# Performance work log

Hardware: AMD Instinct MI355X
Metric: run time of the kernel (lower is better)

The kernel has to match this reference:

```python
import jax, jax.numpy as jnp
import numpy as np
from jax import lax

NPOINT = 1024
RADIUS = 0.4
NSAMPLE = 32
BN_EPS = 1e-5


def _square_distance(src, dst):
    # src [B,S,3], dst [B,N,3] -> [B,S,N]
    d = -2.0 * jnp.einsum('bsc,bnc->bsn', src, dst)
    d = d + jnp.sum(src ** 2, -1)[:, :, None]
    d = d + jnp.sum(dst ** 2, -1)[:, None, :]
    return d


def _farthest_point_sample(xyz, npoint):
    # xyz [B,N,3] -> int32 indices [B,npoint]
    B, N, _ = xyz.shape
    # deterministic start at index 0 (torch uses randint; math is otherwise identical)
    init_far = jnp.zeros((B,), dtype=jnp.int32)
    init_dist = jnp.full((B, N), 1e10, dtype=xyz.dtype)

    def step(carry, _):
        distance, farthest = carry
        centroid = jnp.take_along_axis(xyz, farthest[:, None, None], axis=1)  # [B,1,3]
        dist = jnp.sum((xyz - centroid) ** 2, -1)  # [B,N]
        distance = jnp.minimum(distance, dist)
        new_far = jnp.argmax(distance, axis=-1).astype(jnp.int32)
        return (distance, new_far), farthest

    (_, _), cents = lax.scan(step, (init_dist, init_far), None, length=npoint)
    return cents.T  # [B, npoint]


def _query_ball_point(radius, nsample, xyz, new_xyz):
    # xyz [B,N,3], new_xyz [B,S,3] -> idx [B,S,nsample]
    B, N, _ = xyz.shape
    sqr = _square_distance(new_xyz, xyz)  # [B,S,N]
    ar = jnp.arange(N, dtype=jnp.int32)
    gi = jnp.where(sqr > radius * radius, N, ar[None, None, :])
    gi = jnp.sort(gi, axis=-1)[:, :, :nsample]
    first = gi[:, :, :1]
    return jnp.where(gi == N, first, gi)


def setup_inputs() -> dict:
    key = jax.random.key(0)
    ks = jax.random.split(key, 8)
    B, N = 16, 4096
    inp = {
        'xyz': jax.random.normal(ks[0], (B, 3, N), jnp.float32),
        'points': jax.random.normal(ks[1], (B, 6, N), jnp.float32),
    }
    dims = [(64, 9), (64, 64), (128, 64)]
    for i, (o, c) in enumerate(dims):
        inp[f'w{i}'] = jax.random.normal(ks[2 + i], (o, c), jnp.float32) * 0.05
        inp[f'b{i}'] = jnp.zeros((o,), jnp.float32)
        inp[f'g{i}'] = jnp.ones((o,), jnp.float32)
        inp[f'beta{i}'] = jnp.zeros((o,), jnp.float32)
    return inp


def reference(xyz, points, w0, b0, g0, beta0, w1, b1, g1, beta1, w2, b2, g2, beta2):
    # xyz [B,3,N], points [B,6,N]
    xyz_t = jnp.transpose(xyz, (0, 2, 1))      # [B,N,3]
    pts_t = jnp.transpose(points, (0, 2, 1))   # [B,N,6]
    B, N, _ = xyz_t.shape
    S, ns = NPOINT, NSAMPLE

    fps_idx = _farthest_point_sample(xyz_t, S)                 # [B,S]
    new_xyz = jnp.take_along_axis(xyz_t, fps_idx[:, :, None], axis=1)  # [B,S,3]
    idx = _query_ball_point(RADIUS, ns, xyz_t, new_xyz)        # [B,S,ns]
    flat = idx.reshape(B, S * ns, 1)
    g_xyz = jnp.take_along_axis(xyz_t, flat, axis=1).reshape(B, S, ns, 3)
    g_xyz = g_xyz - new_xyz[:, :, None, :]                     # grouped_xyz_norm
    g_pts = jnp.take_along_axis(pts_t, flat, axis=1).reshape(B, S, ns, -1)
    feat = jnp.concatenate([g_xyz, g_pts], axis=-1)            # [B,S,ns,9]

    # shared MLP: 1x1 conv + BatchNorm (training-mode batch stats) + ReLU
    for w, b, g, be in ((w0, b0, g0, beta0), (w1, b1, g1, beta1), (w2, b2, g2, beta2)):
        h = jnp.einsum('bsnc,oc->bsno', feat, w) + b
        mu = jnp.mean(h, axis=(0, 1, 2))
        var = jnp.var(h, axis=(0, 1, 2))
        feat = jax.nn.relu((h - mu) * lax.rsqrt(var + BN_EPS) * g + be)

    new_points = jnp.max(feat, axis=2)                         # max over nsample -> [B,S,Cout]
    return (jnp.transpose(new_xyz, (0, 2, 1)), jnp.transpose(new_points, (0, 2, 1)))
```

## Files before the change

### kernel.cpp

```cpp
#include <hip/hip_runtime.h>
#include <hip/hip_bf16.h>
#include <stdint.h>

#define NB 16
#define NP 4096
#define NSP 1024
#define KNN 32
#define PTOT (NB*NSP*KNN)
#define NTILES (PTOT/16)

typedef __attribute__((ext_vector_type(8))) short short8;
typedef __attribute__((ext_vector_type(4))) float f32x4;
typedef __attribute__((ext_vector_type(2))) float f32x2;

__device__ __forceinline__ float fadd_(float a,float b){return __fadd_rn(a,b);}
__device__ __forceinline__ float fmul_(float a,float b){return __fmul_rn(a,b);}
__device__ __forceinline__ float fsub_(float a,float b){return __fsub_rn(a,b);}

__device__ __forceinline__ float bf2f(unsigned short u){
    unsigned int x = ((unsigned int)u) << 16; float f; __builtin_memcpy(&f,&x,4); return f;
}
__device__ __forceinline__ unsigned short f2bf(float f){
    unsigned int x; __builtin_memcpy(&x,&f,4);
    x = x + 0x7fffu + ((x>>16)&1u);
    return (unsigned short)(x>>16);
}

template<int CTRL>
__device__ __forceinline__ float dpp_fmax_step(float v){
    int d = __builtin_amdgcn_update_dpp(0, __float_as_int(v), CTRL, 0xF, 0xF, true);
    return fmaxf(v, __int_as_float(d));
}

__global__ __launch_bounds__(256,1) void fps_kernel(const float* __restrict__ xyz,
    int* __restrict__ fps_idx)
{
    const int b = blockIdx.x, tid = threadIdx.x;
    const int lane = tid & 63, wv = tid >> 6;
    const float* xb = xyz + (size_t)b*3*NP;
    __shared__ float4 sp[NP];
    __shared__ unsigned long long slots[2][4];
    f32x2 px[8], py[8], pz[8], pd2[8];
    const int base = tid*16;
#pragma unroll
    for (int j=0;j<16;j+=4){
        float4 vx = *(const float4*)(xb + base + j);
        float4 vy = *(const float4*)(xb + NP + base + j);
        float4 vz = *(const float4*)(xb + 2*NP + base + j);
        px[j/2]   = (f32x2){vx.x,vx.y}; px[j/2+1] = (f32x2){vx.z,vx.w};
        py[j/2]   = (f32x2){vy.x,vy.y}; py[j/2+1] = (f32x2){vy.z,vy.w};
        pz[j/2]   = (f32x2){vz.x,vz.y}; pz[j/2+1] = (f32x2){vz.z,vz.w};
        sp[base+j+0] = make_float4(vx.x,vy.x,vz.x,0.f);
        sp[base+j+1] = make_float4(vx.y,vy.y,vz.y,0.f);
        sp[base+j+2] = make_float4(vx.z,vy.z,vz.z,0.f);
        sp[base+j+3] = make_float4(vx.w,vy.w,vz.w,0.f);
        pd2[j/2]   = (f32x2){1e10f,1e10f};
        pd2[j/2+1] = (f32x2){1e10f,1e10f};
    }
    __syncthreads();
    int far = 0;
    float cx, cy, cz;
    { float4 c0 = sp[0]; cx=c0.x; cy=c0.y; cz=c0.z; }
    for (int s=0;s<NSP;s++){
        if (tid==0) fps_idx[b*NSP+s] = far;
        f32x2 bm2 = (f32x2){-1.f,-1.f};
        {
#pragma clang fp contract(off)
            const f32x2 cx2 = (f32x2){cx,cx}, cy2 = (f32x2){cy,cy}, cz2 = (f32x2){cz,cz};
#pragma unroll
            for (int k=0;k<8;k++){
                f32x2 dx = px[k]-cx2, dy = py[k]-cy2, dz = pz[k]-cz2;
                f32x2 d  = (dx*dx + dy*dy) + dz*dz;
                pd2[k] = __builtin_elementwise_min(pd2[k], d);
                bm2    = __builtin_elementwise_max(bm2, pd2[k]);
            }
        }
        float bd = fmaxf(bm2.x, bm2.y);
        float m = bd;
        m = dpp_fmax_step<0x111>(m);
        m = dpp_fmax_step<0x112>(m);
        m = dpp_fmax_step<0x114>(m);
        m = dpp_fmax_step<0x118>(m);
        m = dpp_fmax_step<0x142>(m);
        m = dpp_fmax_step<0x143>(m);
        const float wm = __int_as_float(__builtin_amdgcn_readlane(__float_as_int(m), 63));
        int il = 0;
#pragma unroll
        for (int k=7;k>=0;k--){
            if (pd2[k].y == wm) il = 2*k+1;
            if (pd2[k].x == wm) il = 2*k;
        }
        unsigned long long wmask = __ballot(bd == wm);
        int L = __ffsll(wmask) - 1;
        int widx = __builtin_amdgcn_readlane(base + il, L);
        unsigned long long key = ((unsigned long long)__float_as_uint(wm) << 32)
                               | (unsigned int)(NP-1-widx);
        if (lane==0) slots[s&1][wv] = key;
        __syncthreads();
        {
            const unsigned long long* sl = slots[s&1];
            unsigned long long a0 = sl[0], a1 = sl[1], a2 = sl[2], a3 = sl[3];
            unsigned long long m0 = a0>a1?a0:a1, m1 = a2>a3?a2:a3;
            unsigned long long mm = m0>m1?m0:m1;
            far = NP-1-(int)(mm & 0xFFFFFFFFu);
        }
        float4 c = sp[far]; cx=c.x; cy=c.y; cz=c.z;
    }
}

__global__ void centroid_kernel(const float* __restrict__ xyz, const int* __restrict__ fps_idx,
    float* __restrict__ new_xyz, float* __restrict__ out0)
{
    int t = blockIdx.x*256 + threadIdx.x;
    if (t >= NB*NSP) return;
    int b = t>>10, s = t&1023;
    int id = fps_idx[t];
    const float* xb = xyz + (size_t)b*3*NP;
    float x=xb[id], y=xb[NP+id], z=xb[2*NP+id];
    float* nz = new_xyz + (size_t)t*3;
    nz[0]=x; nz[1]=y; nz[2]=z;
    out0[(size_t)b*3*NSP + s]         = x;
    out0[(size_t)b*3*NSP + NSP + s]   = y;
    out0[(size_t)b*3*NSP + 2*NSP + s] = z;
}

__global__ __launch_bounds__(256,1) void ball_gather_kernel(const float* __restrict__ xyz,
    const float* __restrict__ pts, const float* __restrict__ new_xyz,
    unsigned short* __restrict__ feat)
{
    const int lane = threadIdx.x & 63, wv = threadIdx.x >> 6;
    const int center = blockIdx.x*4 + wv;
    const int b = center >> 10;
    const float* xb = xyz + (size_t)b*3*NP;
    const float* pb = pts + (size_t)b*6*NP;
    const float* nz = new_xyz + (size_t)center*3;
    const float cx=nz[0], cy=nz[1], cz=nz[2];
    const float src2 = fadd_(fadd_(fmul_(cx,cx),fmul_(cy,cy)),fmul_(cz,cz));
    const float R2 = (float)(0.4*0.4);
    __shared__ int slots[4][32];
    int total = 0;
    for (int c0=0;c0<NP;c0+=64){
        const int i = c0 + lane;
        float x=xb[i], y=xb[NP+i], z=xb[2*NP+i];
        float dot  = fadd_(fadd_(fmul_(cx,x),fmul_(cy,y)),fmul_(cz,z));
        float dst2 = fadd_(fadd_(fmul_(x,x),fmul_(y,y)),fmul_(z,z));
        float d = fadd_(fadd_(fmul_(-2.0f,dot), src2), dst2);
        bool pred = !(d > R2);
        unsigned long long m = __ballot(pred);
        int pos = total + (int)__popcll(m & ((1ull<<lane)-1ull));
        if (pred && pos < 32) slots[wv][pos] = i;
        total += (int)__popcll(m);
        if (total >= 32) break;
    }
    const int nvalid = total < 32 ? total : 32;
    const int n = lane & 31;
    const int idx = slots[wv][ (n < nvalid) ? n : 0 ];
    unsigned short* fr = feat + (size_t)center*KNN*32 + (size_t)n*32;
    if (lane < 32){
        float gx = fsub_(xb[idx], cx), gy = fsub_(xb[NP+idx], cy), gz = fsub_(xb[2*NP+idx], cz);
        float p0=pb[idx], p1=pb[NP+idx], p2=pb[2*NP+idx], p3=pb[3*NP+idx], p4=pb[4*NP+idx];
        short8 v;
        v[0]=(short)f2bf(gx); v[1]=(short)f2bf(gy); v[2]=(short)f2bf(gz);
        v[3]=(short)f2bf(p0); v[4]=(short)f2bf(p1); v[5]=(short)f2bf(p2);
        v[6]=(short)f2bf(p3); v[7]=(short)f2bf(p4);
        *(short8*)fr = v;
    } else {
        float p5 = pb[5*NP+idx];
        short8 v = (short8){0,0,0,0,0,0,0,0};
        v[0]=(short)f2bf(p5);
        *(short8*)(fr+8)  = v;
        short8 z8 = (short8){0,0,0,0,0,0,0,0};
        *(short8*)(fr+16) = z8;
        *(short8*)(fr+24) = z8;
    }
}

template<int KT,int OT,bool NORM_IN,bool STORE_H>
__global__ __launch_bounds__(256,1) void conv_kernel(const unsigned short* __restrict__ in,
    const unsigned short* __restrict__ wp, const float* __restrict__ bias,
    const float* __restrict__ nAB, unsigned short* __restrict__ h_out,
    double* __restrict__ stats)
{
    constexpr int K = KT*32, O = OT*16;
    const int lane = threadIdx.x & 63, wv = threadIdx.x >> 6;
    const int col = lane & 15, quad = lane >> 4;
    short8 bf[OT][KT];
#pragma unroll
    for (int t=0;t<OT;t++)
#pragma unroll
        for (int kt=0;kt<KT;kt++)
            bf[t][kt] = *(const short8*)(wp + (size_t)(t*16+col)*K + kt*32 + quad*8);
    float brow[OT];
#pragma unroll
    for (int t=0;t<OT;t++) brow[t] = bias[t*16+col];
    float nA[KT*8], nB[KT*8];
    if constexpr (NORM_IN){
#pragma unroll
        for (int kt=0;kt<KT;kt++)
#pragma unroll
            for (int j=0;j<8;j++){
                int c = kt*32+quad*8+j;
                nA[kt*8+j]=nAB[c]; nB[kt*8+j]=nAB[128+c];
            }
    }
    float ssum[OT], ssq[OT];
#pragma unroll
    for (int t=0;t<OT;t++){ ssum[t]=0.f; ssq[t]=0.f; }
    const int gw = blockIdx.x*4 + wv, nw = gridDim.x*4;
    for (int tile=gw; tile<NTILES; tile+=nw){
        const int row0 = tile*16;
        short8 af[KT];
#pragma unroll
        for (int kt=0;kt<KT;kt++){
            af[kt] = *(const short8*)(in + (size_t)(row0+col)*K + kt*32 + quad*8);
            if constexpr (NORM_IN){
#pragma unroll
                for (int j=0;j<8;j++){
                    float x = bf2f((unsigned short)af[kt][j]);
                    x = fmaxf(x*nA[kt*8+j]+nB[kt*8+j], 0.f);
                    af[kt][j] = (short)f2bf(x);
                }
            }
        }
        f32x4 acc[OT];
#pragma unroll
        for (int t=0;t<OT;t++) acc[t] = (f32x4){0.f,0.f,0.f,0.f};
#pragma unroll
        for (int kt=0;kt<KT;kt++)
#pragma unroll
            for (int t=0;t<OT;t++)
                acc[t] = __builtin_amdgcn_mfma_f32_16x16x32_bf16(af[kt], bf[t][kt], acc[t], 0,0,0);
#pragma unroll
        for (int t=0;t<OT;t++){
#pragma unroll
            for (int r=0;r<4;r++){
                float h = acc[t][r] + brow[t];
                if constexpr (STORE_H)
                    h_out[(size_t)(row0 + quad*4 + r)*O + t*16 + col] = f2bf(h);
                ssum[t] += h; ssq[t] = fmaf(h,h,ssq[t]);
            }
        }
    }
    __shared__ float bsum[128], bssq[128];
    for (int i=threadIdx.x;i<128;i+=256){ bsum[i]=0.f; bssq[i]=0.f; }
    __syncthreads();
#pragma unroll
    for (int t=0;t<OT;t++){
        float v = ssum[t]; v += __shfl_xor(v,16,64); v += __shfl_xor(v,32,64);
        float q = ssq[t];  q += __shfl_xor(q,16,64); q += __shfl_xor(q,32,64);
        if (quad==0){ atomicAdd(&bsum[t*16+col], v); atomicAdd(&bssq[t*16+col], q); }
    }
    __syncthreads();
    if ((int)threadIdx.x < O){
        const int slot = blockIdx.x & 7;
        atomicAdd(&stats[(size_t)(slot*2+0)*128 + threadIdx.x], (double)bsum[threadIdx.x]);
        atomicAdd(&stats[(size_t)(slot*2+1)*128 + threadIdx.x], (double)bssq[threadIdx.x]);
    }
}

__global__ void finalize_kernel(const double* __restrict__ stats, const float* __restrict__ g,
    const float* __restrict__ beta, float* __restrict__ AB, int O)
{
    int o = threadIdx.x;
    if (o >= O) return;
    double s=0.0, q=0.0;
#pragma unroll
    for (int slot=0;slot<8;slot++){
        s += stats[(size_t)(slot*2+0)*128+o];
        q += stats[(size_t)(slot*2+1)*128+o];
    }
    const double cnt = (double)PTOT;
    float mean = (float)(s/cnt);
    float var  = (float)(q/cnt - (s/cnt)*(s/cnt));
    float inv  = rsqrtf(var + 1e-5f);
    float A = g[o]*inv;
    AB[o] = A; AB[128+o] = beta[o] - mean*A;
}

__global__ __launch_bounds__(256,1) void conv_final_kernel(const unsigned short* __restrict__ in,
    const unsigned short* __restrict__ wp, const float* __restrict__ bias,
    const float* __restrict__ nABin, const float* __restrict__ nABout,
    float* __restrict__ out1)
{
    constexpr int KT=2, OT=8, K=64;
    const int lane = threadIdx.x & 63, wv = threadIdx.x >> 6;
    const int col = lane & 15, quad = lane >> 4;
    short8 bf[OT][KT];
#pragma unroll
    for (int t=0;t<OT;t++)
#pragma unroll
        for (int kt=0;kt<KT;kt++)
            bf[t][kt] = *(const short8*)(wp + (size_t)(t*16+col)*K + kt*32 + quad*8);
    float brow[OT], oA[OT], oB[OT];
#pragma unroll
    for (int t=0;t<OT;t++){
        brow[t] = bias[t*16+col];
        oA[t] = nABout[t*16+col];
        oB[t] = nABout[128+t*16+col];
    }
    float nA[16], nB[16];
#pragma unroll
    for (int kt=0;kt<2;kt++)
#pragma unroll
        for (int j=0;j<8;j++){
            int c = kt*32+quad*8+j;
            nA[kt*8+j]=nABin[c]; nB[kt*8+j]=nABin[128+c];
        }
    const int gw = blockIdx.x*4 + wv, nw = gridDim.x*4;
    for (int grp=gw; grp<NB*NSP; grp+=nw){
        float vmax[OT];
#pragma unroll
        for (int t=0;t<OT;t++) vmax[t]=0.f;
#pragma unroll
        for (int mt=0; mt<2; mt++){
            const int row0 = grp*32 + mt*16;
            short8 af[KT];
#pragma unroll
            for (int kt=0;kt<2;kt++){
                af[kt] = *(const short8*)(in + (size_t)(row0+col)*K + kt*32 + quad*8);
#pragma unroll
                for (int j=0;j<8;j++){
                    float x = bf2f((unsigned short)af[kt][j]);
                    x = fmaxf(x*nA[kt*8+j]+nB[kt*8+j], 0.f);
                    af[kt][j] = (short)f2bf(x);
                }
            }
            f32x4 acc[OT];
#pragma unroll
            for (int t=0;t<OT;t++) acc[t] = (f32x4){0.f,0.f,0.f,0.f};
#pragma unroll
            for (int kt=0;kt<2;kt++)
#pragma unroll
                for (int t=0;t<OT;t++)
                    acc[t] = __builtin_amdgcn_mfma_f32_16x16x32_bf16(af[kt], bf[t][kt], acc[t], 0,0,0);
#pragma unroll
            for (int t=0;t<OT;t++){
#pragma unroll
                for (int r=0;r<4;r++){
                    float h = acc[t][r] + brow[t];
                    float x = fmaxf(h*oA[t]+oB[t], 0.f);
                    vmax[t] = fmaxf(vmax[t], x);
                }
            }
        }
#pragma unroll
        for (int t=0;t<OT;t++){
            float v = vmax[t];
            v = fmaxf(v, __shfl_xor(v,16,64));
            v = fmaxf(v, __shfl_xor(v,32,64));
            if (quad==0){
                int o = t*16+col, bb = grp>>10, ss = grp&1023;
                out1[((size_t)bb*128+o)*NSP + ss] = v;
            }
        }
    }
}

__global__ void prep_kernel(const float* __restrict__ w0, const float* __restrict__ w1,
    const float* __restrict__ w2, unsigned short* __restrict__ wp0,
    unsigned short* __restrict__ wp1, unsigned short* __restrict__ wp2)
{
    int t = blockIdx.x*256 + threadIdx.x;
    if (t < 64*32){ int o=t>>5, c=t&31; wp0[t] = (c<9) ? f2bf(w0[o*9+c]) : (unsigned short)0; }
    if (t < 64*64)  wp1[t] = f2bf(w1[t]);
    if (t < 128*64) wp2[t] = f2bf(w2[t]);
}

extern "C" void kernel_launch(void* const* d_in, const int* in_sizes, int n_in,
                              void* d_out, int out_size, void* d_ws, size_t ws_size,
                              hipStream_t stream)
{
    (void)in_sizes; (void)n_in; (void)out_size; (void)ws_size;
    const float* xyz = (const float*)d_in[0];
    const float* pts = (const float*)d_in[1];
    const float* w0  = (const float*)d_in[2];
    const float* b0  = (const float*)d_in[3];
    const float* g0  = (const float*)d_in[4];
    const float* be0 = (const float*)d_in[5];
    const float* w1  = (const float*)d_in[6];
    const float* b1  = (const float*)d_in[7];
    const float* g1  = (const float*)d_in[8];
    const float* be1 = (const float*)d_in[9];
    const float* w2  = (const float*)d_in[10];
    const float* b2  = (const float*)d_in[11];
    const float* g2  = (const float*)d_in[12];
    const float* be2 = (const float*)d_in[13];

    char* ws = (char*)d_ws;
    size_t off = 0;
    auto alloc = [&](size_t sz)->char*{ char* p = ws + off; off = (off + sz + 255) & ~(size_t)255; return p; };
    int*            fps_idx = (int*)           alloc((size_t)NB*NSP*4);
    float*          new_xyz = (float*)         alloc((size_t)NB*NSP*3*4);
    unsigned short* wp0     = (unsigned short*)alloc(64*32*2);
    unsigned short* wp1     = (unsigned short*)alloc(64*64*2);
    unsigned short* wp2     = (unsigned short*)alloc(128*64*2);
    double*         stats   = (double*)        alloc((size_t)3*8*2*128*8);
    float*          AB0     = (float*)         alloc(256*4);
    float*          AB1     = (float*)         alloc(256*4);
    float*          AB2     = (float*)         alloc(256*4);
    unsigned short* feat    = (unsigned short*)alloc((size_t)PTOT*32*2);
    unsigned short* h0      = (unsigned short*)alloc((size_t)PTOT*64*2);
    unsigned short* h1      = (unsigned short*)alloc((size_t)PTOT*64*2);

    float* out0 = (float*)d_out;
    float* out1 = out0 + (size_t)NB*3*NSP;

    hipMemsetAsync(stats, 0, (size_t)3*8*2*128*8, stream);
    prep_kernel<<<32,256,0,stream>>>(w0,w1,w2,wp0,wp1,wp2);
    fps_kernel<<<NB,256,0,stream>>>(xyz, fps_idx);
    centroid_kernel<<<(NB*NSP+255)/256,256,0,stream>>>(xyz, fps_idx, new_xyz, out0);
    ball_gather_kernel<<<NB*NSP/4,256,0,stream>>>(xyz, pts, new_xyz, feat);
    conv_kernel<1,4,false,true><<<1024,256,0,stream>>>(feat, wp0, b0, nullptr, h0, stats);
    finalize_kernel<<<1,128,0,stream>>>(stats, g0, be0, AB0, 64);
    conv_kernel<2,4,true,true><<<1024,256,0,stream>>>(h0, wp1, b1, AB0, h1, stats + 2048);
    finalize_kernel<<<1,128,0,stream>>>(stats + 2048, g1, be1, AB1, 64);
    conv_kernel<2,8,true,false><<<1024,256,0,stream>>>(h1, wp2, b2, AB1, nullptr, stats + 4096);
    finalize_kernel<<<1,128,0,stream>>>(stats + 4096, g2, be2, AB2, 128);
    conv_final_kernel<<<2048,256,0,stream>>>(h1, wp2, b2, AB1, AB2, out1);
}
```

Measured before the change: 882.0 us.

## Carry winner coordinates through LDS slots in FPS instead of indexed LDS lookup

Each FPS iteration used to reduce the argmax key across waves and then do a dependent LDS read of the full point table to fetch the new centroid. Now every thread selects its local best point's coordinates from registers before the wave reduction. The winning lane writes its key and coordinates together to LDS, so the serial chain loses one dependent LDS load and the 64KB point table goes away. Per-iteration global stores of fps indices are buffered in LDS and written out at the end, at the cost of more register selects per iteration.

```diff
diff --git a/kernel.cpp b/kernel.cpp
--- a/kernel.cpp
+++ b/kernel.cpp
@@ -32,14 +32,27 @@
     return fmaxf(v, __int_as_float(d));
 }
 
+__device__ __forceinline__ float sel16(const f32x2 (&r)[8], int il){
+    const bool b3 = il & 8, b2 = il & 4, b1 = il & 2, b0 = il & 1;
+    f32x2 a0 = b3 ? r[4] : r[0];
+    f32x2 a1 = b3 ? r[5] : r[1];
+    f32x2 a2 = b3 ? r[6] : r[2];
+    f32x2 a3 = b3 ? r[7] : r[3];
+    f32x2 c0 = b2 ? a2 : a0;
+    f32x2 c1 = b2 ? a3 : a1;
+    f32x2 d0 = b1 ? c1 : c0;
+    return b0 ? d0.y : d0.x;
+}
+
 __global__ __launch_bounds__(256,1) void fps_kernel(const float* __restrict__ xyz,
     int* __restrict__ fps_idx)
 {
     const int b = blockIdx.x, tid = threadIdx.x;
     const int lane = tid & 63, wv = tid >> 6;
     const float* xb = xyz + (size_t)b*3*NP;
-    __shared__ float4 sp[NP];
-    __shared__ unsigned long long slots[2][4];
+    __shared__ unsigned long long skey[2][4];
+    __shared__ float4 scoord[2][4];
+    __shared__ int lds_far[NSP];
     f32x2 px[8], py[8], pz[8], pd2[8];
     const int base = tid*16;
 #pragma unroll
@@ -50,19 +63,13 @@
         px[j/2]   = (f32x2){vx.x,vx.y}; px[j/2+1] = (f32x2){vx.z,vx.w};
         py[j/2]   = (f32x2){vy.x,vy.y}; py[j/2+1] = (f32x2){vy.z,vy.w};
         pz[j/2]   = (f32x2){vz.x,vz.y}; pz[j/2+1] = (f32x2){vz.z,vz.w};
-        sp[base+j+0] = make_float4(vx.x,vy.x,vz.x,0.f);
-        sp[base+j+1] = make_float4(vx.y,vy.y,vz.y,0.f);
-        sp[base+j+2] = make_float4(vx.z,vy.z,vz.z,0.f);
-        sp[base+j+3] = make_float4(vx.w,vy.w,vz.w,0.f);
         pd2[j/2]   = (f32x2){1e10f,1e10f};
         pd2[j/2+1] = (f32x2){1e10f,1e10f};
     }
-    __syncthreads();
     int far = 0;
-    float cx, cy, cz;
-    { float4 c0 = sp[0]; cx=c0.x; cy=c0.y; cz=c0.z; }
+    float cx = xb[0], cy = xb[NP], cz = xb[2*NP];
     for (int s=0;s<NSP;s++){
-        if (tid==0) fps_idx[b*NSP+s] = far;
+        if ((s & 255) == tid) lds_far[s] = far;
         f32x2 bm2 = (f32x2){-1.f,-1.f};
         {
 #pragma clang fp contract(off)
@@ -83,29 +90,40 @@
         m = dpp_fmax_step<0x118>(m);
         m = dpp_fmax_step<0x142>(m);
         m = dpp_fmax_step<0x143>(m);
+        int il = 0;
+#pragma unroll
+        for (int k=7;k>=0;k--){
+            if (pd2[k].y == bd) il = 2*k+1;
+            if (pd2[k].x == bd) il = 2*k;
+        }
+        float xv = sel16(px, il), yv = sel16(py, il), zv = sel16(pz, il);
         const float wm = __int_as_float(__builtin_amdgcn_readlane(__float_as_int(m), 63));
-        int il = 0;
-#pragma unroll
-        for (int k=7;k>=0;k--){
-            if (pd2[k].y == wm) il = 2*k+1;
-            if (pd2[k].x == wm) il = 2*k;
-        }
         unsigned long long wmask = __ballot(bd == wm);
-        int L = __ffsll(wmask) - 1;
-        int widx = __builtin_amdgcn_readlane(base + il, L);
-        unsigned long long key = ((unsigned long long)__float_as_uint(wm) << 32)
-                               | (unsigned int)(NP-1-widx);
-        if (lane==0) slots[s&1][wv] = key;
+        bool iwin = (bd == wm) && ((wmask & ((1ull<<lane)-1ull)) == 0);
+        if (iwin){
+            int widx = base + il;
+            skey[s&1][wv] = ((unsigned long long)__float_as_uint(wm) << 32)
+                          | (unsigned int)(NP-1-widx);
+            scoord[s&1][wv] = make_float4(xv, yv, zv, 0.f);
+        }
         __syncthreads();
         {
-            const unsigned long long* sl = slots[s&1];
-            unsigned long long a0 = sl[0], a1 = sl[1], a2 = sl[2], a3 = sl[3];
-            unsigned long long m0 = a0>a1?a0:a1, m1 = a2>a3?a2:a3;
-            unsigned long long mm = m0>m1?m0:m1;
+            const unsigned long long* kk = skey[s&1];
+            const float4* cc = scoord[s&1];
+            unsigned long long k0=kk[0], k1=kk[1], k2=kk[2], k3=kk[3];
+            float4 c0=cc[0], c1=cc[1], c2=cc[2], c3=cc[3];
+            bool g01 = k0 > k1, g23 = k2 > k3;
+            unsigned long long m0 = g01?k0:k1, m1 = g23?k2:k3;
+            float4 q0 = g01?c0:c1, q1 = g23?c2:c3;
+            bool gg = m0 > m1;
+            unsigned long long mm = gg?m0:m1;
+            float4 qq = gg?q0:q1;
             far = NP-1-(int)(mm & 0xFFFFFFFFu);
-        }
-        float4 c = sp[far]; cx=c.x; cy=c.y; cz=c.z;
-    }
+            cx = qq.x; cy = qq.y; cz = qq.z;
+        }
+    }
+    __syncthreads();
+    for (int i=tid;i<NSP;i+=256) fps_idx[b*NSP+i] = lds_far[i];
 }
 
 __global__ void centroid_kernel(const float* __restrict__ xyz, const int* __restrict__ fps_idx,
```

Result: slower. 1.509 ms (+71.1%).

## Process two batches per FPS block to interleave serial reduction latency

Applied to the files above, without the earlier changes.

The farthest-point-sampling kernel now handles two batches per workgroup, interleaving their distance updates, DPP max reductions and barrier per iteration so the two latency chains overlap. Selected indices are buffered in shared memory and written to global memory once at the end instead of per iteration. This halves the number of blocks and doubles register and LDS use per block, so per-iteration work grows while the serial barrier chain is shared.

```diff
diff --git a/kernel.cpp b/kernel.cpp
--- a/kernel.cpp
+++ b/kernel.cpp
@@ -35,76 +35,126 @@
 __global__ __launch_bounds__(256,1) void fps_kernel(const float* __restrict__ xyz,
     int* __restrict__ fps_idx)
 {
-    const int b = blockIdx.x, tid = threadIdx.x;
+    const int blk = blockIdx.x, tid = threadIdx.x;
     const int lane = tid & 63, wv = tid >> 6;
-    const float* xb = xyz + (size_t)b*3*NP;
-    __shared__ float4 sp[NP];
-    __shared__ unsigned long long slots[2][4];
-    f32x2 px[8], py[8], pz[8], pd2[8];
+    const int bA = 2*blk, bB = 2*blk+1;
+    const float* xA = xyz + (size_t)bA*3*NP;
+    const float* xB = xyz + (size_t)bB*3*NP;
+    __shared__ float4 spA[NP];
+    __shared__ float4 spB[NP];
+    __shared__ unsigned long long skA[2][4], skB[2][4];
+    __shared__ int farsA[NSP], farsB[NSP];
+    f32x2 pxA[8], pyA[8], pzA[8], pdA[8];
+    f32x2 pxB[8], pyB[8], pzB[8], pdB[8];
     const int base = tid*16;
 #pragma unroll
     for (int j=0;j<16;j+=4){
-        float4 vx = *(const float4*)(xb + base + j);
-        float4 vy = *(const float4*)(xb + NP + base + j);
-        float4 vz = *(const float4*)(xb + 2*NP + base + j);
-        px[j/2]   = (f32x2){vx.x,vx.y}; px[j/2+1] = (f32x2){vx.z,vx.w};
-        py[j/2]   = (f32x2){vy.x,vy.y}; py[j/2+1] = (f32x2){vy.z,vy.w};
-        pz[j/2]   = (f32x2){vz.x,vz.y}; pz[j/2+1] = (f32x2){vz.z,vz.w};
-        sp[base+j+0] = make_float4(vx.x,vy.x,vz.x,0.f);
-        sp[base+j+1] = make_float4(vx.y,vy.y,vz.y,0.f);
-        sp[base+j+2] = make_float4(vx.z,vy.z,vz.z,0.f);
-        sp[base+j+3] = make_float4(vx.w,vy.w,vz.w,0.f);
-        pd2[j/2]   = (f32x2){1e10f,1e10f};
-        pd2[j/2+1] = (f32x2){1e10f,1e10f};
+        float4 vx = *(const float4*)(xA + base + j);
+        float4 vy = *(const float4*)(xA + NP + base + j);
+        float4 vz = *(const float4*)(xA + 2*NP + base + j);
+        pxA[j/2]   = (f32x2){vx.x,vx.y}; pxA[j/2+1] = (f32x2){vx.z,vx.w};
+        pyA[j/2]   = (f32x2){vy.x,vy.y}; pyA[j/2+1] = (f32x2){vy.z,vy.w};
+        pzA[j/2]   = (f32x2){vz.x,vz.y}; pzA[j/2+1] = (f32x2){vz.z,vz.w};
+        spA[base+j+0] = make_float4(vx.x,vy.x,vz.x,0.f);
+        spA[base+j+1] = make_float4(vx.y,vy.y,vz.y,0.f);
+        spA[base+j+2] = make_float4(vx.z,vy.z,vz.z,0.f);
+        spA[base+j+3] = make_float4(vx.w,vy.w,vz.w,0.f);
+        pdA[j/2]   = (f32x2){1e10f,1e10f};
+        pdA[j/2+1] = (f32x2){1e10f,1e10f};
+    }
+#pragma unroll
+    for (int j=0;j<16;j+=4){
+        float4 vx = *(const float4*)(xB + base + j);
+        float4 vy = *(const float4*)(xB + NP + base + j);
+        float4 vz = *(const float4*)(xB + 2*NP + base + j);
+        pxB[j/2]   = (f32x2){vx.x,vx.y}; pxB[j/2+1] = (f32x2){vx.z,vx.w};
+        pyB[j/2]   = (f32x2){vy.x,vy.y}; pyB[j/2+1] = (f32x2){vy.z,vy.w};
+        pzB[j/2]   = (f32x2){vz.x,vz.y}; pzB[j/2+1] = (f32x2){vz.z,vz.w};
+        spB[base+j+0] = make_float4(vx.x,vy.x,vz.x,0.f);
+        spB[base+j+1] = make_float4(vx.y,vy.y,vz.y,0.f);
+        spB[base+j+2] = make_float4(vx.z,vy.z,vz.z,0.f);
+        spB[base+j+3] = make_float4(vx.w,vy.w,vz.w,0.f);
+        pdB[j/2]   = (f32x2){1e10f,1e10f};
+        pdB[j/2+1] = (f32x2){1e10f,1e10f};
     }
     __syncthreads();
-    int far = 0;
-    float cx, cy, cz;
-    { float4 c0 = sp[0]; cx=c0.x; cy=c0.y; cz=c0.z; }
+    int farA = 0, farB = 0;
+    float cxA = xA[0], cyA = xA[NP], czA = xA[2*NP];
+    float cxB = xB[0], cyB = xB[NP], czB = xB[2*NP];
     for (int s=0;s<NSP;s++){
-        if (tid==0) fps_idx[b*NSP+s] = far;
-        f32x2 bm2 = (f32x2){-1.f,-1.f};
+        if (tid == (s & 255)){ farsA[s] = farA; farsB[s] = farB; }
+        f32x2 bmA = (f32x2){-1.f,-1.f}, bmB = (f32x2){-1.f,-1.f};
         {
 #pragma clang fp contract(off)
-            const f32x2 cx2 = (f32x2){cx,cx}, cy2 = (f32x2){cy,cy}, cz2 = (f32x2){cz,cz};
+            const f32x2 cxA2 = (f32x2){cxA,cxA}, cyA2 = (f32x2){cyA,cyA}, czA2 = (f32x2){czA,czA};
 #pragma unroll
             for (int k=0;k<8;k++){
-                f32x2 dx = px[k]-cx2, dy = py[k]-cy2, dz = pz[k]-cz2;
+                f32x2 dx = pxA[k]-cxA2, dy = pyA[k]-cyA2, dz = pzA[k]-czA2;
                 f32x2 d  = (dx*dx + dy*dy) + dz*dz;
-                pd2[k] = __builtin_elementwise_min(pd2[k], d);
-                bm2    = __builtin_elementwise_max(bm2, pd2[k]);
-            }
-        }
-        float bd = fmaxf(bm2.x, bm2.y);
-        float m = bd;
-        m = dpp_fmax_step<0x111>(m);
-        m = dpp_fmax_step<0x112>(m);
-        m = dpp_fmax_step<0x114>(m);
-        m = dpp_fmax_step<0x118>(m);
-        m = dpp_fmax_step<0x142>(m);
-        m = dpp_fmax_step<0x143>(m);
-        const float wm = __int_as_float(__builtin_amdgcn_readlane(__float_as_int(m), 63));
-        int il = 0;
+                pdA[k] = __builtin_elementwise_min(pdA[k], d);
+                bmA    = __builtin_elementwise_max(bmA, pdA[k]);
+            }
+            const f32x2 cxB2 = (f32x2){cxB,cxB}, cyB2 = (f32x2){cyB,cyB}, czB2 = (f32x2){czB,czB};
+#pragma unroll
+            for (int k=0;k<8;k++){
+                f32x2 dx = pxB[k]-cxB2, dy = pyB[k]-cyB2, dz = pzB[k]-czB2;
+                f32x2 d  = (dx*dx + dy*dy) + dz*dz;
+                pdB[k] = __builtin_elementwise_min(pdB[k], d);
+                bmB    = __builtin_elementwise_max(bmB, pdB[k]);
+            }
+        }
+        float bdA = fmaxf(bmA.x, bmA.y);
+        float bdB = fmaxf(bmB.x, bmB.y);
+        float mA = bdA, mB = bdB;
+        mA = dpp_fmax_step<0x111>(mA); mB = dpp_fmax_step<0x111>(mB);
+        mA = dpp_fmax_step<0x112>(mA); mB = dpp_fmax_step<0x112>(mB);
+        mA = dpp_fmax_step<0x114>(mA); mB = dpp_fmax_step<0x114>(mB);
+        mA = dpp_fmax_step<0x118>(mA); mB = dpp_fmax_step<0x118>(mB);
+        mA = dpp_fmax_step<0x142>(mA); mB = dpp_fmax_step<0x142>(mB);
+        mA = dpp_fmax_step<0x143>(mA); mB = dpp_fmax_step<0x143>(mB);
+        const float wmA = __int_as_float(__builtin_amdgcn_readlane(__float_as_int(mA), 63));
+        const float wmB = __int_as_float(__builtin_amdgcn_readlane(__float_as_int(mB), 63));
+        int ilA = 0, ilB = 0;
 #pragma unroll
         for (int k=7;k>=0;k--){
-            if (pd2[k].y == wm) il = 2*k+1;
-            if (pd2[k].x == wm) il = 2*k;
-        }
-        unsigned long long wmask = __ballot(bd == wm);
-        int L = __ffsll(wmask) - 1;
-        int widx = __builtin_amdgcn_readlane(base + il, L);
-        unsigned long long key = ((unsigned long long)__float_as_uint(wm) << 32)
-                               | (unsigned int)(NP-1-widx);
-        if (lane==0) slots[s&1][wv] = key;
+            if (pdA[k].y == bdA) ilA = 2*k+1;
+            if (pdA[k].x == bdA) ilA = 2*k;
+            if (pdB[k].y == bdB) ilB = 2*k+1;
+            if (pdB[k].x == bdB) ilB = 2*k;
+        }
+        unsigned long long mkA = __ballot(bdA == wmA);
+        unsigned long long mkB = __ballot(bdB == wmB);
+        int LA = __ffsll(mkA) - 1, LB = __ffsll(mkB) - 1;
+        int wiA = __builtin_amdgcn_readlane(base + ilA, LA);
+        int wiB = __builtin_amdgcn_readlane(base + ilB, LB);
+        if (lane==0){
+            skA[s&1][wv] = ((unsigned long long)__float_as_uint(wmA) << 32)
+                         | (unsigned int)(NP-1-wiA);
+            skB[s&1][wv] = ((unsigned long long)__float_as_uint(wmB) << 32)
+                         | (unsigned int)(NP-1-wiB);
+        }
         __syncthreads();
         {
-            const unsigned long long* sl = slots[s&1];
-            unsigned long long a0 = sl[0], a1 = sl[1], a2 = sl[2], a3 = sl[3];
-            unsigned long long m0 = a0>a1?a0:a1, m1 = a2>a3?a2:a3;
-            unsigned long long mm = m0>m1?m0:m1;
-            far = NP-1-(int)(mm & 0xFFFFFFFFu);
-        }
-        float4 c = sp[far]; cx=c.x; cy=c.y; cz=c.z;
+            const unsigned long long* sa = skA[s&1];
+            const unsigned long long* sb = skB[s&1];
+            unsigned long long a0=sa[0], a1=sa[1], a2=sa[2], a3=sa[3];
+            unsigned long long b0=sb[0], b1=sb[1], b2=sb[2], b3=sb[3];
+            unsigned long long am0 = a0>a1?a0:a1, am1 = a2>a3?a2:a3;
+            unsigned long long bm0 = b0>b1?b0:b1, bm1 = b2>b3?b2:b3;
+            unsigned long long amx = am0>am1?am0:am1;
+            unsigned long long bmx = bm0>bm1?bm0:bm1;
+            farA = NP-1-(int)(amx & 0xFFFFFFFFu);
+            farB = NP-1-(int)(bmx & 0xFFFFFFFFu);
+        }
+        float4 cA = spA[farA];
+        float4 cB = spB[farB];
+        cxA=cA.x; cyA=cA.y; czA=cA.z;
+        cxB=cB.x; cyB=cB.y; czB=cB.z;
+    }
+    __syncthreads();
+    for (int i=tid;i<NSP;i+=256){
+        fps_idx[bA*NSP+i] = farsA[i];
+        fps_idx[bB*NSP+i] = farsB[i];
     }
 }
 
@@ -407,7 +457,7 @@
 
     hipMemsetAsync(stats, 0, (size_t)3*8*2*128*8, stream);
     prep_kernel<<<32,256,0,stream>>>(w0,w1,w2,wp0,wp1,wp2);
-    fps_kernel<<<NB,256,0,stream>>>(xyz, fps_idx);
+    fps_kernel<<<NB/2,256,0,stream>>>(xyz, fps_idx);
     centroid_kernel<<<(NB*NSP+255)/256,256,0,stream>>>(xyz, fps_idx, new_xyz, out0);
     ball_gather_kernel<<<NB*NSP/4,256,0,stream>>>(xyz, pts, new_xyz, feat);
     conv_kernel<1,4,false,true><<<1024,256,0,stream>>>(feat, wp0, b0, nullptr, h0, stats);
```

After: 1.310 ms. 1.49x slower.
